# Performance work log

Measured on AMD Instinct MI355X. Metric: run time of the kernel, lower is better.

Reference implementation:

```python
import jax, jax.numpy as jnp
import numpy as np
import math

D_MODEL = 768
EXPAND = 2
D_INNER = D_MODEL * EXPAND  # 1536
D_CONV = 4
D_STATE = 16
DT_RANK = math.ceil(D_MODEL / 16)  # 48
B, L = 2, 2048
LN_EPS = 1e-5


def setup_inputs() -> dict:
    key = jax.random.key(0)
    ks = jax.random.split(key, 12)
    s = lambda fan_in: 1.0 / np.sqrt(fan_in)
    return {
        "x": jax.random.normal(ks[0], (B, L, D_MODEL), dtype=jnp.float32),
        "ln_w": jnp.ones((D_MODEL,), jnp.float32),
        "ln_b": jnp.zeros((D_MODEL,), jnp.float32),
        "in_proj_w": jax.random.normal(ks[1], (2 * D_INNER, D_MODEL), jnp.float32) * s(D_MODEL),
        "conv_w": jax.random.normal(ks[2], (D_INNER, D_CONV), jnp.float32) * s(D_CONV),
        "conv_b": jax.random.normal(ks[3], (D_INNER,), jnp.float32) * 0.01,
        "x_proj_w": jax.random.normal(ks[4], (DT_RANK + 2 * D_STATE, D_INNER), jnp.float32) * s(D_INNER),
        "dt_proj_w": jax.random.normal(ks[5], (D_INNER, DT_RANK), jnp.float32) * s(DT_RANK),
        "dt_proj_b": jax.random.normal(ks[6], (D_INNER,), jnp.float32) * 0.01,
        "A_log": jnp.log(jnp.broadcast_to(jnp.arange(1, D_STATE + 1, dtype=jnp.float32), (D_INNER, D_STATE))),
        "D": jnp.ones((D_INNER,), jnp.float32),
        "out_proj_w": jax.random.normal(ks[7], (D_MODEL, D_INNER), jnp.float32) * s(D_INNER),
    }


def _layernorm(x, w, b):
    mu = jnp.mean(x, axis=-1, keepdims=True)
    var = jnp.mean(jnp.square(x - mu), axis=-1, keepdims=True)
    return (x - mu) * jax.lax.rsqrt(var + LN_EPS) * w + b


def _selective_scan(u, delta, A, Bm, Cm, Dv):
    # u,delta: [b,l,d]; A: [d,n]; Bm,Cm: [b,l,n]; Dv: [d]
    deltaA = jnp.exp(delta[..., None] * A)               # [b,l,d,n]
    dBu = (delta * u)[..., None] * Bm[:, :, None, :]     # [b,l,d,n]
    b, l, d, n = deltaA.shape
    x0 = jnp.zeros((b, d, n), deltaA.dtype)

    def step(carry, inp):
        dA_i, dBu_i, C_i = inp                            # [b,d,n],[b,d,n],[b,n]
        x_new = dA_i * carry + dBu_i
        y_i = jnp.einsum('bdn,bn->bd', x_new, C_i)
        return x_new, y_i

    _, ys = jax.lax.scan(
        step, x0,
        (deltaA.transpose(1, 0, 2, 3), dBu.transpose(1, 0, 2, 3), Cm.transpose(1, 0, 2)))
    y = ys.transpose(1, 0, 2)                             # [b,l,d]
    return y + u * Dv


def reference(x, ln_w, ln_b, in_proj_w, conv_w, conv_b, x_proj_w,
              dt_proj_w, dt_proj_b, A_log, D, out_proj_w):
    residual = x
    h = _layernorm(x, ln_w, ln_b)
    xr = h @ in_proj_w.T                                  # [b,l,2*d_inner]
    u, res = jnp.split(xr, [D_INNER], axis=-1)
    # depthwise causal conv1d
    uc = u.transpose(0, 2, 1)                             # [b,d,l]
    uc = jax.lax.conv_general_dilated(
        uc, conv_w[:, None, :], window_strides=(1,),
        padding=[(D_CONV - 1, 0)],
        dimension_numbers=('NCH', 'OIH', 'NCH'),
        feature_group_count=D_INNER) + conv_b[None, :, None]
    u = jax.nn.silu(uc.transpose(0, 2, 1))                # [b,l,d]
    # SSM
    x_dbl = u @ x_proj_w.T
    dt, Bm, Cm = jnp.split(x_dbl, [DT_RANK, DT_RANK + D_STATE], axis=-1)
    delta = jax.nn.softplus(dt @ dt_proj_w.T + dt_proj_b)
    A = -jnp.exp(A_log)
    y = _selective_scan(u, delta, A, Bm, Cm, D)
    y = y * jax.nn.silu(res)
    return y @ out_proj_w.T + residual
```

## Files before the change

### kernel.cpp

```cpp
#include <hip/hip_runtime.h>

#define DEV __device__ __forceinline__

typedef __attribute__((ext_vector_type(8))) short bf16x8;
typedef __attribute__((ext_vector_type(4))) float f32x4;

#define BB 2
#define LL 2048
#define MM 4096
#define DMODEL 768
#define DINNER 1536
#define NSTATE 16
#define CH 32
#define NCH 64

DEV unsigned short f2b(float f) {
  unsigned int x = __float_as_uint(f);
  x += 0x7fffu + ((x >> 16) & 1u);
  return (unsigned short)(x >> 16);
}
DEV float b2f(unsigned short u) { return __uint_as_float(((unsigned int)u) << 16); }
DEV float silu_f(float v) { return v / (1.f + __expf(-v)); }

DEV void async16(void* lds, const void* g) {
  __builtin_amdgcn_global_load_lds(
      (const __attribute__((address_space(1))) unsigned int*)g,
      (__attribute__((address_space(3))) unsigned int*)lds, 16, 0, 0);
}

__global__ __launch_bounds__(256) void k_prepln(const float* __restrict__ x,
                                                const float* __restrict__ ln_w,
                                                const float* __restrict__ ln_b,
                                                unsigned short* __restrict__ h,
                                                const float* __restrict__ w_in,
                                                const float* __restrict__ w_out,
                                                const float* __restrict__ w_xp,
                                                const float* __restrict__ w_dt,
                                                const float* __restrict__ alog,
                                                unsigned short* __restrict__ winb,
                                                unsigned short* __restrict__ woutb,
                                                unsigned short* __restrict__ wxpb,
                                                unsigned short* __restrict__ wdtb,
                                                float* __restrict__ a2) {
  int bid0 = blockIdx.x, t = threadIdx.x;
  if (bid0 < 4096) {
    int row = bid0;
    const float* xr = x + (size_t)row * DMODEL;
    float v0 = xr[t], v1 = xr[t + 256], v2 = xr[t + 512];
    float s = v0 + v1 + v2;
    float s2 = v0 * v0 + v1 * v1 + v2 * v2;
#pragma unroll
    for (int o = 32; o > 0; o >>= 1) { s += __shfl_down(s, o); s2 += __shfl_down(s2, o); }
    __shared__ float ps[4], ps2[4];
    if ((t & 63) == 0) { ps[t >> 6] = s; ps2[t >> 6] = s2; }
    __syncthreads();
    s = ps[0] + ps[1] + ps[2] + ps[3];
    s2 = ps2[0] + ps2[1] + ps2[2] + ps2[3];
    float mu = s * (1.f / DMODEL);
    float var = s2 * (1.f / DMODEL) - mu * mu;
    float rs = rsqrtf(var + 1e-5f);
    h[(size_t)row * DMODEL + t]       = f2b((v0 - mu) * rs * ln_w[t] + ln_b[t]);
    h[(size_t)row * DMODEL + t + 256] = f2b((v1 - mu) * rs * ln_w[t + 256] + ln_b[t + 256]);
    h[(size_t)row * DMODEL + t + 512] = f2b((v2 - mu) * rs * ln_w[t + 512] + ln_b[t + 512]);
    return;
  }
  int bid = bid0 - 4096;
  if (bid < 2304) {
    int i = bid * 256 + t;
    float4 v = ((const float4*)w_in)[i];
    ushort4 o; o.x = f2b(v.x); o.y = f2b(v.y); o.z = f2b(v.z); o.w = f2b(v.w);
    ((ushort4*)winb)[i] = o;
  } else if (bid < 3456) {
    int i = (bid - 2304) * 256 + t;
    float4 v = ((const float4*)w_out)[i];
    ushort4 o; o.x = f2b(v.x); o.y = f2b(v.y); o.z = f2b(v.z); o.w = f2b(v.w);
    ((ushort4*)woutb)[i] = o;
  } else if (bid < 4224) {
    int i = (bid - 3456) * 256 + t;
    wxpb[i] = (i < 80 * 1536) ? f2b(w_xp[i]) : (unsigned short)0;
  } else if (bid < 4608) {
    int i = (bid - 4224) * 256 + t;
    int row = i >> 6, col = i & 63;
    wdtb[i] = (col < 48) ? f2b(w_dt[row * 48 + col]) : (unsigned short)0;
  } else {
    int i = (bid - 4608) * 256 + t;
    a2[i] = -__expf(alog[i]) * 1.44269504088896f;
  }
}

template <int EPI, int OBF>
__global__ __launch_bounds__(256) void k_gemm_bt(const unsigned short* __restrict__ A,
                                                 const unsigned short* __restrict__ B,
                                                 float* __restrict__ C,
                                                 unsigned short* __restrict__ Cb,
                                                 int M, int N, int Kst, int KC,
                                                 int NBN, int NBM,
                                                 const float* __restrict__ aux) {
  __shared__ unsigned short lA[2][128 * 32];
  __shared__ unsigned short lB[2][128 * 32];
  const int tid = threadIdx.x;
  const int nwg = gridDim.x;
  const int sid = (blockIdx.x & 7) * (nwg >> 3) + (blockIdx.x >> 3);
  const int bn = (sid % NBN) * 128;
  const int t2 = sid / NBN;
  const int bm = (t2 % NBM) * 128;
  const int z = t2 / NBM;
  const int lane = tid & 63;
  const int w = tid >> 6;
  const int wr = (w >> 1) * 64;
  const int wc = (w & 1) * 64;

  f32x4 acc[4][4];
#pragma unroll
  for (int i = 0; i < 4; ++i)
#pragma unroll
    for (int j = 0; j < 4; ++j) acc[i][j] = (f32x4)(0.0f);

  const int srow = tid >> 2;
  const int sg = ((tid & 3) ^ ((srow >> 2) & 3)) * 8;
  const int k0 = z * KC;

#define STAGE_BT(buf, kt)                                                   \
  do {                                                                      \
    _Pragma("unroll") for (int s_ = 0; s_ < 2; ++s_) {                      \
      int row_ = s_ * 64 + srow;                                            \
      int f_ = s_ * 256 + tid;                                              \
      async16(&lA[buf][f_ * 8], A + (size_t)(bm + row_) * Kst + (kt) + sg); \
      async16(&lB[buf][f_ * 8], B + (size_t)(bn + row_) * Kst + (kt) + sg); \
    }                                                                       \
  } while (0)

  STAGE_BT(0, k0);
  asm volatile("s_waitcnt vmcnt(0)" ::: "memory");
  __builtin_amdgcn_s_barrier();

  const int nt = KC >> 5;
  int cur = 0;
  for (int t = 0; t < nt; ++t) {
    if (t + 1 < nt) STAGE_BT(cur ^ 1, k0 + (t + 1) * 32);
    const int ll = lane & 15, sl = lane >> 4;
    bf16x8 af[4], bfr[4];
#pragma unroll
    for (int mi = 0; mi < 4; ++mi) {
      int row = wr + mi * 16 + ll;
      af[mi] = *(const bf16x8*)&lA[cur][row * 32 + ((sl ^ ((row >> 2) & 3)) * 8)];
    }
#pragma unroll
    for (int ni = 0; ni < 4; ++ni) {
      int row = wc + ni * 16 + ll;
      bfr[ni] = *(const bf16x8*)&lB[cur][row * 32 + ((sl ^ ((row >> 2) & 3)) * 8)];
    }
#pragma unroll
    for (int mi = 0; mi < 4; ++mi)
#pragma unroll
      for (int ni = 0; ni < 4; ++ni)
        acc[mi][ni] = __builtin_amdgcn_mfma_f32_16x16x32_bf16(af[mi], bfr[ni], acc[mi][ni], 0, 0, 0);
    asm volatile("s_waitcnt vmcnt(0)" ::: "memory");
    __builtin_amdgcn_s_barrier();
    cur ^= 1;
  }
#undef STAGE_BT

  const size_t zoff = (size_t)z * M * N;
  const int ll = lane & 15, lh4 = (lane >> 4) * 4;
#pragma unroll
  for (int mi = 0; mi < 4; ++mi) {
#pragma unroll
    for (int ni = 0; ni < 4; ++ni) {
      int col = bn + wc + ni * 16 + ll;
#pragma unroll
      for (int q = 0; q < 4; ++q) {
        int row = bm + wr + mi * 16 + lh4 + q;
        size_t idx = (size_t)row * N + col;
        float v = acc[mi][ni][q];
        if (EPI == 1) { v += aux[col]; v = (v > 20.f) ? v : __logf(1.f + __expf(v)); }
        if (OBF) Cb[idx] = f2b(v);
        else C[zoff + idx] = v;
      }
    }
  }
}

__global__ __launch_bounds__(256) void k_gemm64(const unsigned short* __restrict__ A,
                                                const unsigned short* __restrict__ B,
                                                float* __restrict__ C,
                                                int M, int N, int Kst, int KC,
                                                int NBN, int NBM) {
  __shared__ unsigned short lA[2][64 * 32];
  __shared__ unsigned short lB[2][128 * 32];
  const int tid = threadIdx.x;
  const int nwg = gridDim.x;
  const int sid = (blockIdx.x & 7) * (nwg >> 3) + (blockIdx.x >> 3);
  const int bn = (sid % NBN) * 128;
  const int t2 = sid / NBN;
  const int bm = (t2 % NBM) * 64;
  const int z = t2 / NBM;
  const int lane = tid & 63;
  const int w = tid >> 6;
  const int wr = (w >> 1) * 32;
  const int wc = (w & 1) * 64;

  f32x4 acc[2][4];
#pragma unroll
  for (int i = 0; i < 2; ++i)
#pragma unroll
    for (int j = 0; j < 4; ++j) acc[i][j] = (f32x4)(0.0f);

  const int srow = tid >> 2;
  const int sg = ((tid & 3) ^ ((srow >> 2) & 3)) * 8;
  const int k0 = z * KC;

#define STAGE_64(buf, kt)                                                    \
  do {                                                                       \
    async16(&lA[buf][tid * 8], A + (size_t)(bm + srow) * Kst + (kt) + sg);   \
    _Pragma("unroll") for (int i_ = 0; i_ < 2; ++i_) {                       \
      int f_ = i_ * 256 + tid;                                               \
      int r_ = f_ >> 2;                                                      \
      int g_ = ((f_ & 3) ^ ((r_ >> 2) & 3)) * 8;                             \
      async16(&lB[buf][f_ * 8], B + (size_t)(bn + r_) * Kst + (kt) + g_);    \
    }                                                                        \
  } while (0)

  STAGE_64(0, k0);
  asm volatile("s_waitcnt vmcnt(0)" ::: "memory");
  __builtin_amdgcn_s_barrier();

  const int nt = KC >> 5;
  int cur = 0;
  for (int t = 0; t < nt; ++t) {
    if (t + 1 < nt) STAGE_64(cur ^ 1, k0 + (t + 1) * 32);
    const int ll = lane & 15, sl = lane >> 4;
    bf16x8 af[2], bfr[4];
#pragma unroll
    for (int mi = 0; mi < 2; ++mi) {
      int row = wr + mi * 16 + ll;
      af[mi] = *(const bf16x8*)&lA[cur][row * 32 + ((sl ^ ((row >> 2) & 3)) * 8)];
    }
#pragma unroll
    for (int ni = 0; ni < 4; ++ni) {
      int row = wc + ni * 16 + ll;
      bfr[ni] = *(const bf16x8*)&lB[cur][row * 32 + ((sl ^ ((row >> 2) & 3)) * 8)];
    }
#pragma unroll
    for (int mi = 0; mi < 2; ++mi)
#pragma unroll
      for (int ni = 0; ni < 4; ++ni)
        acc[mi][ni] = __builtin_amdgcn_mfma_f32_16x16x32_bf16(af[mi], bfr[ni], acc[mi][ni], 0, 0, 0);
    asm volatile("s_waitcnt vmcnt(0)" ::: "memory");
    __builtin_amdgcn_s_barrier();
    cur ^= 1;
  }
#undef STAGE_64

  const size_t zoff = (size_t)z * M * N;
  const int ll = lane & 15, lh4 = (lane >> 4) * 4;
#pragma unroll
  for (int mi = 0; mi < 2; ++mi) {
#pragma unroll
    for (int ni = 0; ni < 4; ++ni) {
      int col = bn + wc + ni * 16 + ll;
#pragma unroll
      for (int q = 0; q < 4; ++q) {
        int row = bm + wr + mi * 16 + lh4 + q;
        C[zoff + (size_t)row * N + col] = acc[mi][ni][q];
      }
    }
  }
}

__global__ __launch_bounds__(128) void k_xpj_fin(const float* __restrict__ part,
                                                 float* __restrict__ xdbl,
                                                 unsigned short* __restrict__ dtb) {
  int row = blockIdx.x, t = threadIdx.x;
  size_t idx = (size_t)row * 128 + t;
  float s = 0.f;
#pragma unroll
  for (int p = 0; p < 8; ++p) s += part[(size_t)p * MM * 128 + idx];
  xdbl[idx] = s;
  if (t < 64) dtb[row * 64 + t] = (t < 48) ? f2b(s) : (unsigned short)0;
}

__global__ __launch_bounds__(256) void k_opj_fin(const float* __restrict__ part,
                                                 const float* __restrict__ x,
                                                 float* __restrict__ out) {
  int i = blockIdx.x * 256 + threadIdx.x;
  f32x4 a = ((const f32x4*)part)[i];
  f32x4 b = ((const f32x4*)(part + (size_t)MM * DMODEL))[i];
  f32x4 r = ((const f32x4*)x)[i];
  ((f32x4*)out)[i] = a + b + r;
}

__global__ __launch_bounds__(256) void k_conv(const unsigned short* __restrict__ xrb,
                                              const float* __restrict__ cw,
                                              const float* __restrict__ cb,
                                              unsigned short* __restrict__ ub) {
  int i = blockIdx.x * 256 + threadIdx.x;
  int d4 = i % (DINNER / 4);
  int m = i / (DINNER / 4);
  int l = m & (LL - 1);
  const f32x4* cw4 = (const f32x4*)cw;
  f32x4 w0 = cw4[d4 * 4 + 0], w1 = cw4[d4 * 4 + 1];
  f32x4 w2 = cw4[d4 * 4 + 2], w3 = cw4[d4 * 4 + 3];
  f32x4 acc = ((const f32x4*)cb)[d4];
#pragma unroll
  for (int j = 0; j < 4; ++j) {
    if (l - 3 + j >= 0) {
      ushort4 in = ((const ushort4*)(xrb + (size_t)(m - 3 + j) * 3072))[d4];
      f32x4 iv;
      iv[0] = b2f(in.x); iv[1] = b2f(in.y); iv[2] = b2f(in.z); iv[3] = b2f(in.w);
      f32x4 wj;
      wj[0] = w0[j]; wj[1] = w1[j]; wj[2] = w2[j]; wj[3] = w3[j];
      acc += iv * wj;
    }
  }
  ushort4 ob;
  ob.x = f2b(silu_f(acc[0])); ob.y = f2b(silu_f(acc[1]));
  ob.z = f2b(silu_f(acc[2])); ob.w = f2b(silu_f(acc[3]));
  ((ushort4*)ub)[i] = ob;
}

__global__ __launch_bounds__(256) void k_scan1(const unsigned short* __restrict__ deltab,
                                               const unsigned short* __restrict__ ub,
                                               const float* __restrict__ xdbl,
                                               const float* __restrict__ a2g,
                                               float* __restrict__ P, float* __restrict__ S) {
  __shared__ unsigned short sd[CH * 256];
  __shared__ unsigned short su[CH * 256];
  int bid = blockIdx.x;
  int dblk = bid % 6;
  int c = (bid / 6) % NCH;
  int b = bid / (6 * NCH);
  int t = threadIdx.x;
  int d0 = dblk * 256, d = d0 + t;
  size_t mbase = (size_t)b * LL + c * CH;
#pragma unroll
  for (int i = 0; i < 4; ++i) {
    int o = i * 256 + t, r = o >> 5, l = o & 31;
    async16(&sd[r * 256 + l * 8], deltab + (mbase + r) * DINNER + d0 + l * 8);
    async16(&su[r * 256 + l * 8], ub + (mbase + r) * DINNER + d0 + l * 8);
  }
  f32x4 a2v[4], xs[4], pr[4];
  const f32x4* ga = (const f32x4*)(a2g + (size_t)d * 16);
#pragma unroll
  for (int q = 0; q < 4; ++q) { a2v[q] = ga[q]; xs[q] = (f32x4)(0.f); pr[q] = (f32x4)(1.f); }
  __syncthreads();

#pragma unroll 4
  for (int s = 0; s < CH; ++s) {
    float dt = b2f(sd[s * 256 + t]);
    float du = dt * b2f(su[s * 256 + t]);
    const f32x4* gb = (const f32x4*)(xdbl + (mbase + s) * 128 + 48);
#pragma unroll
    for (int q = 0; q < 4; ++q) {
      f32x4 bv = gb[q];
      f32x4 e = dt * a2v[q];
      f32x4 dA;
#pragma unroll
      for (int k = 0; k < 4; ++k) dA[k] = __builtin_amdgcn_exp2f(e[k]);
      xs[q] = dA * xs[q] + du * bv;
      pr[q] = pr[q] * dA;
    }
  }
  size_t base = (size_t)(b * NCH + c) * (16 * DINNER) + d;
#pragma unroll
  for (int q = 0; q < 4; ++q)
#pragma unroll
    for (int k = 0; k < 4; ++k) {
      P[base + (size_t)(q * 4 + k) * DINNER] = pr[q][k];
      S[base + (size_t)(q * 4 + k) * DINNER] = xs[q][k];
    }
}

__global__ __launch_bounds__(256) void k_scan2(float* __restrict__ P, const float* __restrict__ S) {
  int i = blockIdx.x * 256 + threadIdx.x;
  int b = i / (DINNER * 16);
  int j = i % (DINNER * 16);
  const size_t cs = (size_t)DINNER * 16;
  float* Pp = P + (size_t)b * NCH * cs + j;
  const float* Sp = S + (size_t)b * NCH * cs + j;
  float p0[8], s0[8], p1[8], s1[8];
#pragma unroll
  for (int k = 0; k < 8; ++k) { p0[k] = Pp[(size_t)k * cs]; s0[k] = Sp[(size_t)k * cs]; }
#pragma unroll
  for (int k = 0; k < 8; ++k) { p1[k] = Pp[(size_t)(8 + k) * cs]; s1[k] = Sp[(size_t)(8 + k) * cs]; }
  float carry = 0.f;
  for (int g = 0; g < NCH / 8; ++g) {
    float np[8], ns[8];
#pragma unroll
    for (int k = 0; k < 8; ++k) { np[k] = 0.f; ns[k] = 0.f; }
    if (g + 2 < NCH / 8) {
#pragma unroll
      for (int k = 0; k < 8; ++k) {
        np[k] = Pp[(size_t)((g + 2) * 8 + k) * cs];
        ns[k] = Sp[(size_t)((g + 2) * 8 + k) * cs];
      }
    }
#pragma unroll
    for (int k = 0; k < 8; ++k) {
      float tmp = carry;
      carry = fmaf(p0[k], carry, s0[k]);
      Pp[(size_t)(g * 8 + k) * cs] = tmp;
    }
#pragma unroll
    for (int k = 0; k < 8; ++k) { p0[k] = p1[k]; s0[k] = s1[k]; p1[k] = np[k]; s1[k] = ns[k]; }
  }
}

__global__ __launch_bounds__(256) void k_scan3(const unsigned short* __restrict__ deltab,
                                               const unsigned short* __restrict__ ub,
                                               const float* __restrict__ xdbl,
                                               const float* __restrict__ a2g,
                                               const float* __restrict__ P,
                                               const float* __restrict__ Dv,
                                               const unsigned short* __restrict__ xrb,
                                               unsigned short* __restrict__ yb) {
  __shared__ unsigned short sd[CH * 256];
  __shared__ unsigned short su[CH * 256];
  int bid = blockIdx.x;
  int dblk = bid % 6;
  int c = (bid / 6) % NCH;
  int b = bid / (6 * NCH);
  int t = threadIdx.x;
  int d0 = dblk * 256, d = d0 + t;
  size_t mbase = (size_t)b * LL + c * CH;
#pragma unroll
  for (int i = 0; i < 4; ++i) {
    int o = i * 256 + t, r = o >> 5, l = o & 31;
    async16(&sd[r * 256 + l * 8], deltab + (mbase + r) * DINNER + d0 + l * 8);
    async16(&su[r * 256 + l * 8], ub + (mbase + r) * DINNER + d0 + l * 8);
  }
  f32x4 a2v[4], xs[4];
  const f32x4* ga = (const f32x4*)(a2g + (size_t)d * 16);
#pragma unroll
  for (int q = 0; q < 4; ++q) a2v[q] = ga[q];
  size_t base = (size_t)(b * NCH + c) * (16 * DINNER) + d;
#pragma unroll
  for (int q = 0; q < 4; ++q)
#pragma unroll
    for (int k = 0; k < 4; ++k) xs[q][k] = P[base + (size_t)(q * 4 + k) * DINNER];
  float dval = Dv[d];
  __syncthreads();

#pragma unroll 4
  for (int s = 0; s < CH; ++s) {
    size_t m = mbase + s;
    float dt = b2f(sd[s * 256 + t]);
    float uv = b2f(su[s * 256 + t]);
    float du = dt * uv;
    const f32x4* gb = (const f32x4*)(xdbl + m * 128 + 48);
    const f32x4* gc = (const f32x4*)(xdbl + m * 128 + 64);
    f32x4 yv = (f32x4)(0.f);
#pragma unroll
    for (int q = 0; q < 4; ++q) {
      f32x4 bv = gb[q], cv = gc[q];
      f32x4 e = dt * a2v[q];
      f32x4 dA;
#pragma unroll
      for (int k = 0; k < 4; ++k) dA[k] = __builtin_amdgcn_exp2f(e[k]);
      xs[q] = dA * xs[q] + du * bv;
      yv += xs[q] * cv;
    }
    float y = yv[0] + yv[1] + yv[2] + yv[3] + uv * dval;
    float res = b2f(xrb[m * 3072 + DINNER + d]);
    y *= silu_f(res);
    yb[m * DINNER + d] = f2b(y);
  }
}

extern "C" void kernel_launch(void* const* d_in, const int* in_sizes, int n_in,
                              void* d_out, int out_size, void* d_ws, size_t ws_size,
                              hipStream_t stream) {
  const float* x     = (const float*)d_in[0];
  const float* ln_w  = (const float*)d_in[1];
  const float* ln_b  = (const float*)d_in[2];
  const float* w_in  = (const float*)d_in[3];
  const float* cw    = (const float*)d_in[4];
  const float* cb    = (const float*)d_in[5];
  const float* w_xp  = (const float*)d_in[6];
  const float* w_dt  = (const float*)d_in[7];
  const float* b_dt  = (const float*)d_in[8];
  const float* alog  = (const float*)d_in[9];
  const float* Dv    = (const float*)d_in[10];
  const float* w_out = (const float*)d_in[11];
  float* out = (float*)d_out;

  char* ws = (char*)d_ws;
  unsigned short* h_b    = (unsigned short*)(ws + 0);
  unsigned short* winb   = (unsigned short*)(ws + 6291456);
  unsigned short* woutb  = (unsigned short*)(ws + 11010048);
  unsigned short* wxpb   = (unsigned short*)(ws + 13369344);
  unsigned short* wdtb   = (unsigned short*)(ws + 13762560);
  float*          a2     = (float*)(ws + 13959168);
  unsigned short* xrb    = (unsigned short*)(ws + 14057472);
  unsigned short* ub     = (unsigned short*)(ws + 39223296);
  float*          xpart  = (float*)(ws + 51806208);
  float*          xdbl   = (float*)(ws + 68583424);
  unsigned short* dtb    = (unsigned short*)(ws + 70680576);
  unsigned short* deltab = (unsigned short*)(ws + 71204864);
  float*          P      = (float*)(ws + 83787776);
  float*          S      = (float*)(ws + 96370688);
  unsigned short* yb     = (unsigned short*)(ws + 108953600);
  float*          opart  = (float*)(ws + 121536512);

  k_prepln<<<8800, 256, 0, stream>>>(x, ln_w, ln_b, h_b, w_in, w_out, w_xp, w_dt, alog,
                                     winb, woutb, wxpb, wdtb, a2);

  k_gemm_bt<0, 1><<<768, 256, 0, stream>>>(h_b, winb, nullptr, xrb, MM, 3072, 768, 768, 24, 32, nullptr);

  k_conv<<<(MM * (DINNER / 4)) / 256, 256, 0, stream>>>(xrb, cw, cb, ub);

  k_gemm_bt<0, 0><<<256, 256, 0, stream>>>(ub, wxpb, xpart, nullptr, MM, 128, 1536, 192, 1, 32, nullptr);
  k_xpj_fin<<<MM, 128, 0, stream>>>(xpart, xdbl, dtb);

  k_gemm_bt<1, 1><<<384, 256, 0, stream>>>(dtb, wdtb, nullptr, deltab, MM, DINNER, 64, 64, 12, 32, b_dt);

  k_scan1<<<BB * NCH * 6, 256, 0, stream>>>(deltab, ub, xdbl, a2, P, S);
  k_scan2<<<(BB * DINNER * 16) / 256, 256, 0, stream>>>(P, S);
  k_scan3<<<BB * NCH * 6, 256, 0, stream>>>(deltab, ub, xdbl, a2, P, Dv, xrb, yb);

  k_gemm64<<<768, 256, 0, stream>>>(yb, woutb, opart, MM, DMODEL, 1536, 768, 6, 64);
  k_opj_fin<<<(MM * DMODEL / 4) / 256, 256, 0, stream>>>(opart, x, out);
}
```

Baseline: 161.9 us.

## Fuse residual add into out-proj GEMM, drop split-K, move gate SiLU into in-proj epilogue

The out-projection GEMM no longer uses split-K with a separate reduction kernel. It runs a single pass over the full K and adds the residual in its epilogue, which removes the partial-sum buffer round trip and one launch. The gate SiLU moves from the scan's output stage into the in-projection GEMM's bf16 epilogue for the upper half of the columns. s_setprio is also raised around the MFMA blocks. The trade-off is half as many workgroups (384) for the out-projection, each doing a longer K loop, which lowers parallelism.

```diff
diff --git a/kernel.cpp b/kernel.cpp
--- a/kernel.cpp
+++ b/kernel.cpp
@@ -88,7 +88,7 @@
   }
 }
 
-template <int EPI, int OBF>
+template <int EPI, int OBF, int SILU_HI>
 __global__ __launch_bounds__(256) void k_gemm_bt(const unsigned short* __restrict__ A,
                                                  const unsigned short* __restrict__ B,
                                                  float* __restrict__ C,
@@ -150,11 +150,13 @@
       int row = wc + ni * 16 + ll;
       bfr[ni] = *(const bf16x8*)&lB[cur][row * 32 + ((sl ^ ((row >> 2) & 3)) * 8)];
     }
+    __builtin_amdgcn_s_setprio(1);
 #pragma unroll
     for (int mi = 0; mi < 4; ++mi)
 #pragma unroll
       for (int ni = 0; ni < 4; ++ni)
         acc[mi][ni] = __builtin_amdgcn_mfma_f32_16x16x32_bf16(af[mi], bfr[ni], acc[mi][ni], 0, 0, 0);
+    __builtin_amdgcn_s_setprio(0);
     asm volatile("s_waitcnt vmcnt(0)" ::: "memory");
     __builtin_amdgcn_s_barrier();
     cur ^= 1;
@@ -163,6 +165,7 @@
 
   const size_t zoff = (size_t)z * M * N;
   const int ll = lane & 15, lh4 = (lane >> 4) * 4;
+  const bool hi = SILU_HI && (bn >= DINNER);
 #pragma unroll
   for (int mi = 0; mi < 4; ++mi) {
 #pragma unroll
@@ -174,6 +177,7 @@
         size_t idx = (size_t)row * N + col;
         float v = acc[mi][ni][q];
         if (EPI == 1) { v += aux[col]; v = (v > 20.f) ? v : __logf(1.f + __expf(v)); }
+        if (SILU_HI) { if (hi) v = silu_f(v); }
         if (OBF) Cb[idx] = f2b(v);
         else C[zoff + idx] = v;
       }
@@ -184,17 +188,16 @@
 __global__ __launch_bounds__(256) void k_gemm64(const unsigned short* __restrict__ A,
                                                 const unsigned short* __restrict__ B,
                                                 float* __restrict__ C,
-                                                int M, int N, int Kst, int KC,
-                                                int NBN, int NBM) {
+                                                int M, int N, int Kst,
+                                                int NBN, int NBM,
+                                                const float* __restrict__ aux) {
   __shared__ unsigned short lA[2][64 * 32];
   __shared__ unsigned short lB[2][128 * 32];
   const int tid = threadIdx.x;
   const int nwg = gridDim.x;
   const int sid = (blockIdx.x & 7) * (nwg >> 3) + (blockIdx.x >> 3);
   const int bn = (sid % NBN) * 128;
-  const int t2 = sid / NBN;
-  const int bm = (t2 % NBM) * 64;
-  const int z = t2 / NBM;
+  const int bm = (sid / NBN) * 64;
   const int lane = tid & 63;
   const int w = tid >> 6;
   const int wr = (w >> 1) * 32;
@@ -208,7 +211,6 @@
 
   const int srow = tid >> 2;
   const int sg = ((tid & 3) ^ ((srow >> 2) & 3)) * 8;
-  const int k0 = z * KC;
 
 #define STAGE_64(buf, kt)                                                    \
   do {                                                                       \
@@ -221,14 +223,14 @@
     }                                                                        \
   } while (0)
 
-  STAGE_64(0, k0);
+  STAGE_64(0, 0);
   asm volatile("s_waitcnt vmcnt(0)" ::: "memory");
   __builtin_amdgcn_s_barrier();
 
-  const int nt = KC >> 5;
+  const int nt = Kst >> 5;
   int cur = 0;
   for (int t = 0; t < nt; ++t) {
-    if (t + 1 < nt) STAGE_64(cur ^ 1, k0 + (t + 1) * 32);
+    if (t + 1 < nt) STAGE_64(cur ^ 1, (t + 1) * 32);
     const int ll = lane & 15, sl = lane >> 4;
     bf16x8 af[2], bfr[4];
 #pragma unroll
@@ -241,18 +243,19 @@
       int row = wc + ni * 16 + ll;
       bfr[ni] = *(const bf16x8*)&lB[cur][row * 32 + ((sl ^ ((row >> 2) & 3)) * 8)];
     }
+    __builtin_amdgcn_s_setprio(1);
 #pragma unroll
     for (int mi = 0; mi < 2; ++mi)
 #pragma unroll
       for (int ni = 0; ni < 4; ++ni)
         acc[mi][ni] = __builtin_amdgcn_mfma_f32_16x16x32_bf16(af[mi], bfr[ni], acc[mi][ni], 0, 0, 0);
+    __builtin_amdgcn_s_setprio(0);
     asm volatile("s_waitcnt vmcnt(0)" ::: "memory");
     __builtin_amdgcn_s_barrier();
     cur ^= 1;
   }
 #undef STAGE_64
 
-  const size_t zoff = (size_t)z * M * N;
   const int ll = lane & 15, lh4 = (lane >> 4) * 4;
 #pragma unroll
   for (int mi = 0; mi < 2; ++mi) {
@@ -262,7 +265,8 @@
 #pragma unroll
       for (int q = 0; q < 4; ++q) {
         int row = bm + wr + mi * 16 + lh4 + q;
-        C[zoff + (size_t)row * N + col] = acc[mi][ni][q];
+        size_t idx = (size_t)row * N + col;
+        C[idx] = acc[mi][ni][q] + aux[idx];
       }
     }
   }
@@ -278,16 +282,6 @@
   for (int p = 0; p < 8; ++p) s += part[(size_t)p * MM * 128 + idx];
   xdbl[idx] = s;
   if (t < 64) dtb[row * 64 + t] = (t < 48) ? f2b(s) : (unsigned short)0;
-}
-
-__global__ __launch_bounds__(256) void k_opj_fin(const float* __restrict__ part,
-                                                 const float* __restrict__ x,
-                                                 float* __restrict__ out) {
-  int i = blockIdx.x * 256 + threadIdx.x;
-  f32x4 a = ((const f32x4*)part)[i];
-  f32x4 b = ((const f32x4*)(part + (size_t)MM * DMODEL))[i];
-  f32x4 r = ((const f32x4*)x)[i];
-  ((f32x4*)out)[i] = a + b + r;
 }
 
 __global__ __launch_bounds__(256) void k_conv(const unsigned short* __restrict__ xrb,
@@ -462,7 +456,7 @@
     }
     float y = yv[0] + yv[1] + yv[2] + yv[3] + uv * dval;
     float res = b2f(xrb[m * 3072 + DINNER + d]);
-    y *= silu_f(res);
+    y *= res;
     yb[m * DINNER + d] = f2b(y);
   }
 }
@@ -500,24 +494,22 @@
   float*          P      = (float*)(ws + 83787776);
   float*          S      = (float*)(ws + 96370688);
   unsigned short* yb     = (unsigned short*)(ws + 108953600);
-  float*          opart  = (float*)(ws + 121536512);
 
   k_prepln<<<8800, 256, 0, stream>>>(x, ln_w, ln_b, h_b, w_in, w_out, w_xp, w_dt, alog,
                                      winb, woutb, wxpb, wdtb, a2);
 
-  k_gemm_bt<0, 1><<<768, 256, 0, stream>>>(h_b, winb, nullptr, xrb, MM, 3072, 768, 768, 24, 32, nullptr);
+  k_gemm_bt<0, 1, 1><<<768, 256, 0, stream>>>(h_b, winb, nullptr, xrb, MM, 3072, 768, 768, 24, 32, nullptr);
 
   k_conv<<<(MM * (DINNER / 4)) / 256, 256, 0, stream>>>(xrb, cw, cb, ub);
 
-  k_gemm_bt<0, 0><<<256, 256, 0, stream>>>(ub, wxpb, xpart, nullptr, MM, 128, 1536, 192, 1, 32, nullptr);
+  k_gemm_bt<0, 0, 0><<<256, 256, 0, stream>>>(ub, wxpb, xpart, nullptr, MM, 128, 1536, 192, 1, 32, nullptr);
   k_xpj_fin<<<MM, 128, 0, stream>>>(xpart, xdbl, dtb);
 
-  k_gemm_bt<1, 1><<<384, 256, 0, stream>>>(dtb, wdtb, nullptr, deltab, MM, DINNER, 64, 64, 12, 32, b_dt);
+  k_gemm_bt<1, 1, 0><<<384, 256, 0, stream>>>(dtb, wdtb, nullptr, deltab, MM, DINNER, 64, 64, 12, 32, b_dt);
 
   k_scan1<<<BB * NCH * 6, 256, 0, stream>>>(deltab, ub, xdbl, a2, P, S);
   k_scan2<<<(BB * DINNER * 16) / 256, 256, 0, stream>>>(P, S);
   k_scan3<<<BB * NCH * 6, 256, 0, stream>>>(deltab, ub, xdbl, a2, P, Dv, xrb, yb);
 
-  k_gemm64<<<768, 256, 0, stream>>>(yb, woutb, opart, MM, DMODEL, 1536, 768, 6, 64);
-  k_opj_fin<<<(MM * DMODEL / 4) / 256, 256, 0, stream>>>(opart, x, out);
-}
+  k_gemm64<<<384, 256, 0, stream>>>(yb, woutb, out, MM, DMODEL, 1536, 6, 64, x);
+}
```

Result: no change. 161.5 us (-0.2%).
